# Kernel optimization log

Measured on AMD Instinct MI355X. Metric: run time of the kernel, lower is better.

## Reference

```python
import jax, jax.numpy as jnp
import numpy as np

N = 100000   # nodes
E = 600000   # edges
H = 128      # hidden_size
G = 4000     # graphs in batch
T = 128      # num_tasks
ATOM_DIMS = np.array([119, 5, 12, 12, 10, 6, 6, 2, 2])  # OGB atom feature vocab sizes
OFFSETS = jnp.asarray(np.concatenate([[0], np.cumsum(ATOM_DIMS)[:-1]]), dtype=jnp.int64)


def setup_inputs() -> dict:
    key = jax.random.key(0)
    ks = jax.random.split(key, 12)
    x = jax.random.randint(ks[0], (N, 9), 0, 2)
    edge_index = jax.random.randint(ks[1], (2, E), 0, N)
    batch = jnp.sort(jax.random.randint(ks[2], (N,), 0, G))
    s = 1.0 / np.sqrt(H)
    atom_emb = jax.random.normal(ks[3], (int(ATOM_DIMS.sum()), H), dtype=jnp.float32) * 0.02
    W1 = jax.random.normal(ks[4], (H, H), dtype=jnp.float32) * s
    b1 = jnp.zeros((H,), dtype=jnp.float32)
    W2 = jax.random.normal(ks[5], (H, H), dtype=jnp.float32) * s
    b2 = jnp.zeros((H,), dtype=jnp.float32)
    W3 = jax.random.normal(ks[6], (H, H), dtype=jnp.float32) * s
    b3 = jnp.zeros((H,), dtype=jnp.float32)
    Wl = jax.random.normal(ks[7], (H, T), dtype=jnp.float32) * s
    bl = jnp.zeros((T,), dtype=jnp.float32)
    return dict(x=x, edge_index=edge_index, batch=batch, atom_emb=atom_emb,
                W1=W1, b1=b1, W2=W2, b2=b2, W3=W3, b3=b3, Wl=Wl, bl=bl)


def _gcn_conv(h, W, b, src, dst, dinv):
    # GCNConv: linear transform, then symmetric-normalized scatter-add with self-loops
    h = h @ W                                        # [N,H]
    norm = dinv[src] * dinv[dst]                     # [E]
    msg = h[src] * norm[:, None]                     # [E,H]
    agg = jax.ops.segment_sum(msg, dst, num_segments=N)
    # self-loop contribution: norm_ii = dinv_i^2, weight 1
    return agg + (dinv * dinv)[:, None] * h + b


def reference(x, edge_index, batch, atom_emb, W1, b1, W2, b2, W3, b3, Wl, bl):
    src, dst = edge_index[0], edge_index[1]
    # degree with self-loops (edge_weight = 1)
    deg = jax.ops.segment_sum(jnp.ones((E,), dtype=atom_emb.dtype), dst, num_segments=N) + 1.0
    dinv = jax.lax.rsqrt(deg)
    # AtomEncoder: sum of per-feature embeddings (one concatenated table + offsets)
    h = atom_emb[x + OFFSETS[None, :]].sum(axis=1)   # [N,H]
    h = jax.nn.relu(_gcn_conv(h, W1, b1, src, dst, dinv))
    h = jax.nn.relu(_gcn_conv(h, W2, b2, src, dst, dinv))
    h = _gcn_conv(h, W3, b3, src, dst, dinv)
    # global mean pool over graphs
    cnt = jax.ops.segment_sum(jnp.ones((N,), dtype=h.dtype), batch, num_segments=G)
    pooled = jax.ops.segment_sum(h, batch, num_segments=G) / jnp.maximum(cnt, 1.0)[:, None]
    return pooled @ Wl + bl                          # [G,T]
```

## Files before the change

kernel.cpp:

```cpp
#include <hip/hip_runtime.h>

#define NN 100000
#define EE 600000
#define HH 128
#define GG 4000
#define TT 128
#define PAD 64

typedef short short8 __attribute__((ext_vector_type(8)));
typedef unsigned short ushort8v __attribute__((ext_vector_type(8)));
typedef float floatx4 __attribute__((ext_vector_type(4)));

static __device__ __forceinline__ float bf2f(unsigned short u) {
  union { unsigned int i; float f; } v; v.i = ((unsigned int)u) << 16; return v.f;
}
static __device__ __forceinline__ unsigned short f2bf(float f) {
  union { float f; unsigned int i; } v; v.f = f;
  unsigned int r = (v.i + 0x7FFFu + ((v.i >> 16) & 1u)) >> 16;
  return (unsigned short)r;
}

#define DB ((EE / 4 + 255) / 256)
#define NB ((NN + 255) / 256)
#define AGG_GRID (NN / 16)

__global__ __launch_bounds__(256) void fill_enc_wt_k(const int* __restrict__ ei,
                                                     int* __restrict__ cnt,
                                                     int* __restrict__ csr_pad,
                                                     const int* __restrict__ x,
                                                     const float* __restrict__ emb,
                                                     unsigned short* __restrict__ h0,
                                                     const float* __restrict__ W1,
                                                     const float* __restrict__ W2,
                                                     const float* __restrict__ W3,
                                                     unsigned short* __restrict__ Wt) {
  if (blockIdx.x < DB) {
    int e4 = (blockIdx.x * 256 + threadIdx.x) * 4;
    if (e4 >= EE) return;
    int4 s = *(const int4*)(ei + e4);
    int4 d = *(const int4*)(ei + EE + e4);
    int o0 = atomicAdd(&cnt[d.x], 1);
    int o1 = atomicAdd(&cnt[d.y], 1);
    int o2 = atomicAdd(&cnt[d.z], 1);
    int o3 = atomicAdd(&cnt[d.w], 1);
    if (o0 < PAD) csr_pad[d.x * PAD + o0] = s.x;
    if (o1 < PAD) csr_pad[d.y * PAD + o1] = s.y;
    if (o2 < PAD) csr_pad[d.z * PAD + o2] = s.z;
    if (o3 < PAD) csr_pad[d.w * PAD + o3] = s.w;
  } else if (blockIdx.x < DB + NN / 16) {
    const int lane = threadIdx.x & 63;
    const int wid  = threadIdx.x >> 6;
    const int l16  = lane & 15;
    const int n = (blockIdx.x - DB) * 16 + wid * 4 + (lane >> 4);
    const int off[9] = {0, 119, 124, 136, 148, 158, 164, 170, 172};
    int xv = (l16 < 9) ? x[n * 9 + l16] : 0;
    float s[8] = {0.f, 0.f, 0.f, 0.f, 0.f, 0.f, 0.f, 0.f};
#pragma unroll
    for (int f = 0; f < 9; f++) {
      int idx = __shfl(xv, (lane & 48) | f, 64) + off[f];
      const float* ep = emb + (size_t)idx * HH + l16 * 8;
      float4 e0 = *(const float4*)ep;
      float4 e1 = *(const float4*)(ep + 4);
      s[0] += e0.x; s[1] += e0.y; s[2] += e0.z; s[3] += e0.w;
      s[4] += e1.x; s[5] += e1.y; s[6] += e1.z; s[7] += e1.w;
    }
    ushort8v o;
#pragma unroll
    for (int j = 0; j < 8; j++) o[j] = f2bf(s[j]);
    *(ushort8v*)(h0 + (size_t)n * HH + l16 * 8) = o;
  } else {
    int f = (blockIdx.x - DB - NN / 16) * 256 + threadIdx.x;
    int wsel = f >> 14;
    int r = (f >> 7) & 127;
    int k = f & 127;
    const float* W = (wsel == 0) ? W1 : (wsel == 1) ? W2 : W3;
    Wt[wsel * HH * HH + r * HH + k] = f2bf(W[k * HH + r]);
  }
}

template <bool L1GATHER>
__global__ __launch_bounds__(256) void agg_bf_k(const int* __restrict__ cnt,
                                                const int* __restrict__ csr_pad,
                                                const unsigned short* __restrict__ Hs,
                                                unsigned short* __restrict__ Aggs,
                                                const int* __restrict__ batch,
                                                int* __restrict__ gs) {
  if (L1GATHER && blockIdx.x >= AGG_GRID) {
    const int i = (blockIdx.x - AGG_GRID) * 256 + threadIdx.x;
    if (i < NN) {
      int b0 = batch[i];
      int b1 = (i + 1 < NN) ? batch[i + 1] : GG;
      for (int g = b0 + 1; g <= b1; g++) gs[g] = i + 1;
      if (i == 0)
        for (int g = 0; g <= b0; g++) gs[g] = 0;
    }
    return;
  }
  const int lane = threadIdx.x & 63;
  const int wid  = threadIdx.x >> 6;
  const int l16  = lane & 15;
  const int n = blockIdx.x * 16 + wid * 4 + (lane >> 4);
  const int deg = cnt[n];
  const int beg = n * PAD;
  const int end = beg + deg;
  const int last = end - 1;
  const float dn = rsqrtf((float)deg + 1.0f);
  float acc[8];
  {
    ushort8v v = *(const ushort8v*)(Hs + (size_t)n * HH + l16 * 8);
    const float sw = L1GATHER ? dn : 1.0f;
#pragma unroll
    for (int j = 0; j < 8; j++) acc[j] = sw * bf2f(v[j]);
  }
  int i = beg;
  if (i < end) {
    int c[8];
#pragma unroll
    for (int j = 0; j < 8; j++) c[j] = csr_pad[min(i + j, last)];
    while (true) {
      float m[8];
      m[0] = 1.f;
#pragma unroll
      for (int j = 1; j < 8; j++) m[j] = (i + j < end) ? 1.f : 0.f;
      if (L1GATHER) {
#pragma unroll
        for (int j = 0; j < 8; j++) m[j] *= rsqrtf((float)cnt[c[j]] + 1.0f);
      }
      ushort8v v[8];
#pragma unroll
      for (int j = 0; j < 8; j++)
        v[j] = *(const ushort8v*)(Hs + (size_t)c[j] * HH + l16 * 8);
      const int ni = i + 8;
      int p[8];
      if (ni < end) {
#pragma unroll
        for (int j = 0; j < 8; j++) p[j] = csr_pad[min(ni + j, last)];
      }
#pragma unroll
      for (int j = 0; j < 8; j++)
#pragma unroll
        for (int k = 0; k < 8; k++) acc[k] += m[j] * bf2f(v[j][k]);
      i = ni;
      if (i >= end) break;
#pragma unroll
      for (int j = 0; j < 8; j++) c[j] = p[j];
    }
  }
  ushort8v o;
#pragma unroll
  for (int j = 0; j < 8; j++) o[j] = f2bf(dn * acc[j]);
  *(ushort8v*)(Aggs + (size_t)n * HH + l16 * 8) = o;
}

template <bool LAST>
__global__ __launch_bounds__(256) void gemm_mfma_k(const unsigned short* __restrict__ A,
                                                   const unsigned short* __restrict__ Wt,
                                                   const float* __restrict__ b,
                                                   const int* __restrict__ cnt,
                                                   unsigned short* __restrict__ Out) {
  const int w = threadIdx.x >> 6;
  const int l = threadIdx.x & 63;
  const int m16 = l & 15;
  const int q8  = (l >> 4) * 8;
  const int bm  = blockIdx.x * 128 + w * 32;

  floatx4 acc[2][8];
#pragma unroll
  for (int i = 0; i < 2; i++)
#pragma unroll
    for (int j = 0; j < 8; j++) acc[i][j] = (floatx4){0.f, 0.f, 0.f, 0.f};

  for (int q = 0; q < 4; q++) {
    const int k0 = q * 32;
    short8 a[2];
#pragma unroll
    for (int ti = 0; ti < 2; ti++) {
      int row = bm + ti * 16 + m16;
      a[ti] = (row < NN) ? *(const short8*)(A + (size_t)row * HH + k0 + q8)
                         : (short8){0, 0, 0, 0, 0, 0, 0, 0};
    }
#pragma unroll
    for (int tn = 0; tn < 8; tn++) {
      short8 bf = *(const short8*)(Wt + (size_t)(tn * 16 + m16) * HH + k0 + q8);
      acc[0][tn] = __builtin_amdgcn_mfma_f32_16x16x32_bf16(a[0], bf, acc[0][tn], 0, 0, 0);
      acc[1][tn] = __builtin_amdgcn_mfma_f32_16x16x32_bf16(a[1], bf, acc[1][tn], 0, 0, 0);
    }
  }

  float bias[8];
#pragma unroll
  for (int tn = 0; tn < 8; tn++) bias[tn] = b[tn * 16 + m16];

#pragma unroll
  for (int ti = 0; ti < 2; ti++) {
    const int rbase = bm + ti * 16 + (l >> 4) * 4;
#pragma unroll
    for (int r = 0; r < 4; r++) {
      const int row = rbase + r;
      if (row < NN) {
        const float dv = LAST ? 1.0f : rsqrtf((float)cnt[row] + 1.0f);
#pragma unroll
        for (int tn = 0; tn < 8; tn++) {
          const int col = tn * 16 + m16;
          float v = acc[ti][tn][r] + bias[tn];
          if (!LAST) v = dv * fmaxf(v, 0.f);
          Out[(size_t)row * HH + col] = f2bf(v);
        }
      }
    }
  }
}

__global__ __launch_bounds__(128) void pool_final_k(const int* __restrict__ gs,
                                                    const unsigned short* __restrict__ h3,
                                                    const float* __restrict__ Wl,
                                                    const float* __restrict__ bl,
                                                    float* __restrict__ out) {
  const int g = blockIdx.x;
  const int t = threadIdx.x;
  const int beg = gs[g];
  const int end = gs[g + 1];
  float s = 0.f;
  for (int n = beg; n < end; n++) s += bf2f(h3[(size_t)n * HH + t]);
  __shared__ float p[128];
  p[t] = s / (float)max(end - beg, 1);
  __syncthreads();
  float acc = bl[t];
#pragma unroll 8
  for (int h = 0; h < HH; h++) acc += p[h] * Wl[h * TT + t];
  out[(size_t)g * TT + t] = acc;
}

extern "C" void kernel_launch(void* const* d_in, const int* in_sizes, int n_in,
                              void* d_out, int out_size, void* d_ws, size_t ws_size,
                              hipStream_t stream) {
  const int*   x     = (const int*)d_in[0];
  const int*   ei    = (const int*)d_in[1];
  const int*   batch = (const int*)d_in[2];
  const float* emb   = (const float*)d_in[3];
  const float* W1    = (const float*)d_in[4];
  const float* b1    = (const float*)d_in[5];
  const float* W2    = (const float*)d_in[6];
  const float* b2    = (const float*)d_in[7];
  const float* W3    = (const float*)d_in[8];
  const float* b3    = (const float*)d_in[9];
  const float* Wl    = (const float*)d_in[10];
  const float* bl    = (const float*)d_in[11];
  float* out = (float*)d_out;

  unsigned short* bufA = (unsigned short*)d_ws;
  unsigned short* bufB = bufA + (size_t)NN * HH;
  unsigned short* Wt   = bufB + (size_t)NN * HH;
  int*   cnt    = (int*)(Wt + 3 * HH * HH);
  int*   gs     = cnt + NN;
  int*   csr    = gs + GG + 1;

  hipMemsetAsync(cnt, 0, NN * sizeof(int), stream);

  fill_enc_wt_k<<<DB + NN / 16 + 192, 256, 0, stream>>>(ei, cnt, csr,
                                                        x, emb, bufA,
                                                        W1, W2, W3, Wt);

  const int gemm_grid = (NN + 127) / 128;

  agg_bf_k<true><<<AGG_GRID + NB, 256, 0, stream>>>(cnt, csr, bufA, bufB, batch, gs);
  gemm_mfma_k<false><<<gemm_grid, 256, 0, stream>>>(bufB, Wt, b1, cnt, bufA);

  agg_bf_k<false><<<AGG_GRID, 256, 0, stream>>>(cnt, csr, bufA, bufB, batch, gs);
  gemm_mfma_k<false><<<gemm_grid, 256, 0, stream>>>(bufB, Wt + HH * HH, b2, cnt, bufA);

  agg_bf_k<false><<<AGG_GRID, 256, 0, stream>>>(cnt, csr, bufA, bufB, batch, gs);
  gemm_mfma_k<true><<<gemm_grid, 256, 0, stream>>>(bufB, Wt + 2 * HH * HH, b3, cnt, bufA);

  pool_final_k<<<GG, 128, 0, stream>>>(gs, bufA, Wl, bl, out);
}
```

Baseline: 315.8 us.

## Fold last GCN linear layer into the readout weight and skip the third GEMM

Because the third layer has no activation and mean pooling is linear, W3·Wl and b3·Wl+bl are precomputed into a combined weight and bias inside the setup kernel. Pooling then runs directly on the third aggregation output, and the final full-size GEMM over all nodes is removed. This removes one pass that reads and writes the node-feature matrix. In exchange, a small serial 128x128 matrix product is added to the setup kernel, and the order of rounding changes.

Result: faster. 292.2 us (-7.5%).

```diff
diff --git a/kernel.cpp b/kernel.cpp
--- a/kernel.cpp
+++ b/kernel.cpp
@@ -23,6 +23,9 @@
 #define DB ((EE / 4 + 255) / 256)
 #define NB ((NN + 255) / 256)
 #define AGG_GRID (NN / 16)
+#define ENCB (NN / 16)
+#define WTB 128
+#define WCB 128
 
 __global__ __launch_bounds__(256) void fill_enc_wt_k(const int* __restrict__ ei,
                                                      int* __restrict__ cnt,
@@ -32,8 +35,13 @@
                                                      unsigned short* __restrict__ h0,
                                                      const float* __restrict__ W1,
                                                      const float* __restrict__ W2,
+                                                     unsigned short* __restrict__ Wt,
                                                      const float* __restrict__ W3,
-                                                     unsigned short* __restrict__ Wt) {
+                                                     const float* __restrict__ Wl,
+                                                     const float* __restrict__ b3,
+                                                     const float* __restrict__ bl,
+                                                     float* __restrict__ Wc,
+                                                     float* __restrict__ bc) {
   if (blockIdx.x < DB) {
     int e4 = (blockIdx.x * 256 + threadIdx.x) * 4;
     if (e4 >= EE) return;
@@ -47,7 +55,7 @@
     if (o1 < PAD) csr_pad[d.y * PAD + o1] = s.y;
     if (o2 < PAD) csr_pad[d.z * PAD + o2] = s.z;
     if (o3 < PAD) csr_pad[d.w * PAD + o3] = s.w;
-  } else if (blockIdx.x < DB + NN / 16) {
+  } else if (blockIdx.x < DB + ENCB) {
     const int lane = threadIdx.x & 63;
     const int wid  = threadIdx.x >> 6;
     const int l16  = lane & 15;
@@ -68,13 +76,28 @@
 #pragma unroll
     for (int j = 0; j < 8; j++) o[j] = f2bf(s[j]);
     *(ushort8v*)(h0 + (size_t)n * HH + l16 * 8) = o;
-  } else {
-    int f = (blockIdx.x - DB - NN / 16) * 256 + threadIdx.x;
+  } else if (blockIdx.x < DB + ENCB + WTB) {
+    int f = (blockIdx.x - DB - ENCB) * 256 + threadIdx.x;
     int wsel = f >> 14;
     int r = (f >> 7) & 127;
     int k = f & 127;
-    const float* W = (wsel == 0) ? W1 : (wsel == 1) ? W2 : W3;
+    const float* W = (wsel == 0) ? W1 : W2;
     Wt[wsel * HH * HH + r * HH + k] = f2bf(W[k * HH + r]);
+  } else if (blockIdx.x < DB + ENCB + WTB + WCB) {
+    const int h = blockIdx.x - DB - ENCB - WTB;
+    const int t = threadIdx.x & 127;
+    if (threadIdx.x >= 128) return;
+    float acc = 0.f;
+#pragma unroll 8
+    for (int k = 0; k < HH; k++) acc += W3[h * HH + k] * Wl[k * TT + t];
+    Wc[h * TT + t] = acc;
+  } else {
+    const int t = threadIdx.x & 127;
+    if (threadIdx.x >= 128) return;
+    float acc = bl[t];
+#pragma unroll 8
+    for (int k = 0; k < HH; k++) acc += b3[k] * Wl[k * TT + t];
+    bc[t] = acc;
   }
 }
 
@@ -152,7 +175,6 @@
   *(ushort8v*)(Aggs + (size_t)n * HH + l16 * 8) = o;
 }
 
-template <bool LAST>
 __global__ __launch_bounds__(256) void gemm_mfma_k(const unsigned short* __restrict__ A,
                                                    const unsigned short* __restrict__ Wt,
                                                    const float* __restrict__ b,
@@ -198,12 +220,12 @@
     for (int r = 0; r < 4; r++) {
       const int row = rbase + r;
       if (row < NN) {
-        const float dv = LAST ? 1.0f : rsqrtf((float)cnt[row] + 1.0f);
+        const float dv = rsqrtf((float)cnt[row] + 1.0f);
 #pragma unroll
         for (int tn = 0; tn < 8; tn++) {
           const int col = tn * 16 + m16;
           float v = acc[ti][tn][r] + bias[tn];
-          if (!LAST) v = dv * fmaxf(v, 0.f);
+          v = dv * fmaxf(v, 0.f);
           Out[(size_t)row * HH + col] = f2bf(v);
         }
       }
@@ -212,22 +234,22 @@
 }
 
 __global__ __launch_bounds__(128) void pool_final_k(const int* __restrict__ gs,
-                                                    const unsigned short* __restrict__ h3,
-                                                    const float* __restrict__ Wl,
-                                                    const float* __restrict__ bl,
+                                                    const unsigned short* __restrict__ a3,
+                                                    const float* __restrict__ Wc,
+                                                    const float* __restrict__ bc,
                                                     float* __restrict__ out) {
   const int g = blockIdx.x;
   const int t = threadIdx.x;
   const int beg = gs[g];
   const int end = gs[g + 1];
   float s = 0.f;
-  for (int n = beg; n < end; n++) s += bf2f(h3[(size_t)n * HH + t]);
+  for (int n = beg; n < end; n++) s += bf2f(a3[(size_t)n * HH + t]);
   __shared__ float p[128];
   p[t] = s / (float)max(end - beg, 1);
   __syncthreads();
-  float acc = bl[t];
+  float acc = bc[t];
 #pragma unroll 8
-  for (int h = 0; h < HH; h++) acc += p[h] * Wl[h * TT + t];
+  for (int h = 0; h < HH; h++) acc += p[h] * Wc[h * TT + t];
   out[(size_t)g * TT + t] = acc;
 }
 
@@ -251,26 +273,26 @@
   unsigned short* bufA = (unsigned short*)d_ws;
   unsigned short* bufB = bufA + (size_t)NN * HH;
   unsigned short* Wt   = bufB + (size_t)NN * HH;
-  int*   cnt    = (int*)(Wt + 3 * HH * HH);
+  float* Wc     = (float*)(Wt + 2 * HH * HH);
+  float* bc     = Wc + HH * TT;
+  int*   cnt    = (int*)(bc + TT);
   int*   gs     = cnt + NN;
   int*   csr    = gs + GG + 1;
 
   hipMemsetAsync(cnt, 0, NN * sizeof(int), stream);
 
-  fill_enc_wt_k<<<DB + NN / 16 + 192, 256, 0, stream>>>(ei, cnt, csr,
-                                                        x, emb, bufA,
-                                                        W1, W2, W3, Wt);
+  fill_enc_wt_k<<<DB + ENCB + WTB + WCB + 1, 256, 0, stream>>>(
+      ei, cnt, csr, x, emb, bufA, W1, W2, Wt, W3, Wl, b3, bl, Wc, bc);
 
   const int gemm_grid = (NN + 127) / 128;
 
   agg_bf_k<true><<<AGG_GRID + NB, 256, 0, stream>>>(cnt, csr, bufA, bufB, batch, gs);
-  gemm_mfma_k<false><<<gemm_grid, 256, 0, stream>>>(bufB, Wt, b1, cnt, bufA);
+  gemm_mfma_k<<<gemm_grid, 256, 0, stream>>>(bufB, Wt, b1, cnt, bufA);
 
   agg_bf_k<false><<<AGG_GRID, 256, 0, stream>>>(cnt, csr, bufA, bufB, batch, gs);
-  gemm_mfma_k<false><<<gemm_grid, 256, 0, stream>>>(bufB, Wt + HH * HH, b2, cnt, bufA);
+  gemm_mfma_k<<<gemm_grid, 256, 0, stream>>>(bufB, Wt + HH * HH, b2, cnt, bufA);
 
   agg_bf_k<false><<<AGG_GRID, 256, 0, stream>>>(cnt, csr, bufA, bufB, batch, gs);
-  gemm_mfma_k<true><<<gemm_grid, 256, 0, stream>>>(bufB, Wt + 2 * HH * HH, b3, cnt, bufA);
-
-  pool_final_k<<<GG, 128, 0, stream>>>(gs, bufA, Wl, bl, out);
-}
+
+  pool_final_k<<<GG, 128, 0, stream>>>(gs, bufB, Wc, bc, out);
+}
```
